# Kernel optimization log

Measured on AMD Instinct MI355X. Metric: run time of the kernel, lower is better.

## Reference

```python
import jax, jax.numpy as jnp
import numpy as np
from jax import lax

D_MODEL = 2048
D_INNER = 4096  # expand * d_model
D_CONV = 4
B, T = 4, 2048


def _rmsnorm(h):
    # F.normalize(x, dim=-1) * sqrt(D): x / max(||x||_2, 1e-12) * sqrt(D)
    n = jnp.sqrt(jnp.sum(h * h, axis=-1, keepdims=True))
    return h / jnp.maximum(n, 1e-12) * (h.shape[-1] ** 0.5)


def setup_inputs() -> dict:
    key = jax.random.key(0)
    ks = jax.random.split(key, 7)
    std = 0.02
    return {
        "x": jax.random.normal(ks[0], (B, T, D_MODEL), jnp.float32),
        "W_in": jax.random.normal(ks[1], (2 * D_INNER, D_MODEL), jnp.float32) * std,
        "conv_w": jax.random.normal(ks[2], (D_INNER, 1, D_CONV), jnp.float32) * std,
        "conv_b": jnp.zeros((D_INNER,), jnp.float32),
        "W_out": jax.random.normal(ks[3], (D_MODEL, D_INNER), jnp.float32) * std,
        "W_mlp1": jax.random.normal(ks[4], (4 * D_MODEL, D_MODEL), jnp.float32) * std,
        "W_mlp2": jax.random.normal(ks[5], (D_MODEL, 4 * D_MODEL), jnp.float32) * std,
    }


def _mamba_fallback(h, W_in, conv_w, conv_b, W_out):
    # in_proj: (B,T,D) -> (B,T,2*d_inner), split into x branch and gate z
    xz = jnp.einsum("btd,ed->bte", h, W_in)
    xp, z = jnp.split(xz, 2, axis=-1)
    # depthwise causal conv over time: torch pads (d_conv-1) both sides then slices [:T]
    # == left-pad-only causal cross-correlation
    xc = lax.conv_general_dilated(
        xp.transpose(0, 2, 1),  # (B, d_inner, T)
        conv_w,                  # (d_inner, 1, d_conv)
        window_strides=(1,),
        padding=[(D_CONV - 1, 0)],
        dimension_numbers=("NCH", "OIH", "NCH"),
        feature_group_count=D_INNER,
    ) + conv_b[None, :, None]
    xc = xc.transpose(0, 2, 1)  # (B, T, d_inner)
    y = jax.nn.silu(xc) * jax.nn.silu(z)
    return jnp.einsum("bte,de->btd", y, W_out)


def reference(x, W_in, conv_w, conv_b, W_out, W_mlp1, W_mlp2):
    # full-dimension path (active_dim=None)
    h = _rmsnorm(x)
    x = x + _mamba_fallback(h, W_in, conv_w, conv_b, W_out)
    h = _rmsnorm(x)
    m = jnp.einsum("bte,de->btd", jax.nn.relu(jnp.einsum("btd,ed->bte", h, W_mlp1)), W_mlp2)
    return x + m
```

## Files before the change

### kernel.cpp

```cpp
#include <hip/hip_runtime.h>
#include <hip/hip_bf16.h>

typedef __bf16 bf16;
typedef __bf16 bf16x8 __attribute__((ext_vector_type(8)));
typedef float f32x4 __attribute__((ext_vector_type(4)));

#define D_MODEL 2048
#define D_INNER 4096
#define ROWS    8192

__device__ __forceinline__ void gload_lds16(const void* g, void* l) {
    __builtin_amdgcn_global_load_lds(
        (const __attribute__((address_space(1))) void*)g,
        (__attribute__((address_space(3))) void*)l, 16, 0, 0);
}

__device__ __forceinline__ void f2b_body(const float* __restrict__ in,
                                         bf16* __restrict__ out, int i, int n8) {
    if (i >= n8) return;
    long base = (long)i * 8;
    float4 a = *(const float4*)(in + base);
    float4 b = *(const float4*)(in + base + 4);
    bf16x8 o;
    o[0] = (bf16)a.x; o[1] = (bf16)a.y; o[2] = (bf16)a.z; o[3] = (bf16)a.w;
    o[4] = (bf16)b.x; o[5] = (bf16)b.y; o[6] = (bf16)b.z; o[7] = (bf16)b.w;
    *(bf16x8*)(out + base) = o;
}

__device__ __forceinline__ void rmsnorm_body(const float* __restrict__ x,
                                             bf16* __restrict__ h, int row) {
    const float* xr = x + (long)row * D_MODEL;
    float4 v0 = ((const float4*)xr)[threadIdx.x * 2];
    float4 v1 = ((const float4*)xr)[threadIdx.x * 2 + 1];
    float ss = v0.x*v0.x + v0.y*v0.y + v0.z*v0.z + v0.w*v0.w
             + v1.x*v1.x + v1.y*v1.y + v1.z*v1.z + v1.w*v1.w;
    #pragma unroll
    for (int o = 32; o; o >>= 1) ss += __shfl_xor(ss, o, 64);
    __shared__ float red[4];
    if ((threadIdx.x & 63) == 0) red[threadIdx.x >> 6] = ss;
    __syncthreads();
    float tot = red[0] + red[1] + red[2] + red[3];
    float scale = 45.254834f / fmaxf(sqrtf(tot), 1e-12f);
    bf16x8 o;
    o[0] = (bf16)(v0.x*scale); o[1] = (bf16)(v0.y*scale);
    o[2] = (bf16)(v0.z*scale); o[3] = (bf16)(v0.w*scale);
    o[4] = (bf16)(v1.x*scale); o[5] = (bf16)(v1.y*scale);
    o[6] = (bf16)(v1.z*scale); o[7] = (bf16)(v1.w*scale);
    *(bf16x8*)(h + (long)row * D_MODEL + threadIdx.x * 8) = o;
}

__device__ __forceinline__ void conv_body(bf16* __restrict__ xz,
                                          const float* __restrict__ cw,
                                          const float* __restrict__ cb, int idx) {
    const int c8  = idx & 511;
    const int row = idx >> 9;
    const int t   = row & 2047;
    const int c0  = c8 * 8;
    float acc[8];
    float wv[8][4];
    #pragma unroll
    for (int e = 0; e < 8; ++e) {
        float4 f = ((const float4*)cw)[c0 + e];
        wv[e][0] = f.x; wv[e][1] = f.y; wv[e][2] = f.z; wv[e][3] = f.w;
        acc[e] = cb[c0 + e];
    }
    #pragma unroll
    for (int j = 0; j < 4; ++j) {
        if (t + j - 3 >= 0) {
            bf16x8 xv = *(const bf16x8*)(xz + (long)(row + j - 3) * (2*D_INNER) + c0);
            #pragma unroll
            for (int e = 0; e < 8; ++e) acc[e] += (float)xv[e] * wv[e][j];
        }
    }
    bf16* zp = xz + (long)row * (2*D_INNER) + D_INNER + c0;
    bf16x8 zv = *(const bf16x8*)zp;
    bf16x8 yv;
    #pragma unroll
    for (int e = 0; e < 8; ++e) {
        float xc = acc[e];
        float s1 = xc / (1.f + __expf(-xc));
        float z  = (float)zv[e];
        float s2 = z / (1.f + __expf(-z));
        yv[e] = (bf16)(s1 * s2);
    }
    *(bf16x8*)zp = yv;
}

__global__ __launch_bounds__(256) void prep_kernel(const float* __restrict__ x,
                                                   bf16* __restrict__ h,
                                                   const float* __restrict__ w,
                                                   bf16* __restrict__ wOut, int n8) {
    if ((int)blockIdx.x < ROWS) rmsnorm_body(x, h, blockIdx.x);
    else f2b_body(w, wOut, (blockIdx.x - ROWS) * 256 + threadIdx.x, n8);
}

__global__ __launch_bounds__(256) void convf2b_kernel(bf16* __restrict__ xz,
                                                      const float* __restrict__ cw,
                                                      const float* __restrict__ cb,
                                                      const float* __restrict__ w,
                                                      bf16* __restrict__ wOut, int n8) {
    if ((int)blockIdx.x < 16384) conv_body(xz, cw, cb, blockIdx.x * 256 + threadIdx.x);
    else f2b_body(w, wOut, (blockIdx.x - 16384) * 256 + threadIdx.x, n8);
}

__global__ __launch_bounds__(256) void f2b_kernel(const float* __restrict__ in,
                                                  bf16* __restrict__ out, int n8) {
    f2b_body(in, out, blockIdx.x * 256 + threadIdx.x, n8);
}

template<int EPI>
__global__ __launch_bounds__(512, 2) void gemm_bt(
        const bf16* __restrict__ A, long lda,
        const bf16* __restrict__ B,
        void* __restrict__ C, const float* __restrict__ res,
        int N, int K, int gx) {
    __shared__ __align__(16) char LB[131072];
    const int tid = threadIdx.x;
    const int w   = tid >> 6;
    const int l   = tid & 63;
    const int lr  = l & 15;

    int bx, by;
    if (gx == 32) {
        const int xcd = blockIdx.x & 7, i = blockIdx.x >> 3;
        by = (xcd >> 1) * 8 + (i >> 4);
        bx = (xcd & 1) * 16 + (i & 15);
    } else {
        const int qq = gridDim.x >> 3;
        const int sw = (blockIdx.x & 7) * qq + (blockIdx.x >> 3);
        bx = sw % gx; by = sw / gx;
    }
    const long rowBase = (long)by * 256;
    const long colBase = (long)bx * 256;

    const int srow = w * 8 + (l >> 3);
    const int schk = (l & 7) ^ ((l >> 3) & 7);
    const bf16* aSrc = A + (rowBase + srow) * lda + schk * 8;
    const bf16* bSrc = B + (colBase + srow) * (long)K + schk * 8;
    const long lda64 = 64 * lda;
    const long ldb64 = 64 * (long)K;
    const int  w1024 = w * 1024;

    auto stgA = [&](int DBB, int kt) {
        const bf16* s = aSrc + (long)kt * 64;
        gload_lds16(s,            LB + DBB +     0 + w1024);
        gload_lds16(s +   lda64,  LB + DBB +  8192 + w1024);
        gload_lds16(s + 2*lda64,  LB + DBB + 16384 + w1024);
        gload_lds16(s + 3*lda64,  LB + DBB + 24576 + w1024);
    };
    auto stgB = [&](int DBB, int kt) {
        const bf16* s = bSrc + (long)kt * 64;
        gload_lds16(s,            LB + DBB + 32768 + w1024);
        gload_lds16(s +   ldb64,  LB + DBB + 40960 + w1024);
        gload_lds16(s + 2*ldb64,  LB + DBB + 49152 + w1024);
        gload_lds16(s + 3*ldb64,  LB + DBB + 57344 + w1024);
    };

    const int cx0 = (((l >> 4)    ) ^ (l & 7)) << 4;
    const int cx1 = (((l >> 4) + 4) ^ (l & 7)) << 4;
    const int hm = w >> 2;
    const int q  = w & 3;
    int aRow[8], bRow[4];
    #pragma unroll
    for (int m = 0; m < 8; ++m) aRow[m] = hm * 16384 + (m * 16 + lr) * 128;
    #pragma unroll
    for (int n = 0; n < 4; ++n)
        bRow[n] = 32768 + (q >> 1) * 16384 + ((q & 1) * 64 + n * 16 + lr) * 128;

    const int nt  = K >> 6;
    const int nit = nt >> 1;
    f32x4 acc[8][4] = {};
    bf16x8 AX[4][2], BL[2][2], BH[2][2];

    stgB(0, 0);      stgA(0, 0);
    stgB(65536, 1);  stgA(65536, 1);
    asm volatile("s_waitcnt vmcnt(8)" ::: "memory");
    __builtin_amdgcn_s_barrier();
    __builtin_amdgcn_sched_barrier(0);
    #pragma unroll
    for (int m = 0; m < 4; ++m) {
        AX[m][0] = *(const bf16x8*)(LB + aRow[m] + cx0);
        AX[m][1] = *(const bf16x8*)(LB + aRow[m] + cx1);
    }
    #pragma unroll
    for (int n = 0; n < 2; ++n) {
        BL[n][0] = *(const bf16x8*)(LB + bRow[n]     + cx0);
        BL[n][1] = *(const bf16x8*)(LB + bRow[n]     + cx1);
    }
    #pragma unroll
    for (int n = 0; n < 2; ++n) {
        BH[n][0] = *(const bf16x8*)(LB + bRow[n + 2] + cx0);
        BH[n][1] = *(const bf16x8*)(LB + bRow[n + 2] + cx1);
    }
    asm volatile("s_waitcnt lgkmcnt(4)" ::: "memory");
    __builtin_amdgcn_sched_barrier(0);
    __builtin_amdgcn_s_setprio(1);
    #pragma unroll
    for (int m = 0; m < 4; ++m)
        #pragma unroll
        for (int n = 0; n < 2; ++n) {
            acc[m][n] = __builtin_amdgcn_mfma_f32_16x16x32_bf16(AX[m][0], BL[n][0], acc[m][n], 0, 0, 0);
            acc[m][n] = __builtin_amdgcn_mfma_f32_16x16x32_bf16(AX[m][1], BL[n][1], acc[m][n], 0, 0, 0);
        }
    __builtin_amdgcn_s_setprio(0);
    __builtin_amdgcn_s_barrier();

    for (int it = 0; it < nit; ++it) {
        int kA = 2 * it + 2; if (kA >= nt) kA = 0;
        int kB = 2 * it + 3; if (kB >= nt) kB = 0;
        #pragma unroll
        for (int db = 0; db < 2; ++db) {
            const int DBB = db * 65536;
            const char* Lb = LB + DBB;
            const char* Ln = LB + (DBB ^ 65536);
            const int kst = db ? kB : kA;
            const bool full = (db == 0) || (it < nit - 1);

            stgB(DBB, kst);
            __builtin_amdgcn_s_setprio(1);
            #pragma unroll
            for (int m = 0; m < 4; ++m) {
                #pragma unroll
                for (int n = 0; n < 2; ++n) {
                    acc[m][n + 2] = __builtin_amdgcn_mfma_f32_16x16x32_bf16(AX[m][0], BH[n][0], acc[m][n + 2], 0, 0, 0);
                    acc[m][n + 2] = __builtin_amdgcn_mfma_f32_16x16x32_bf16(AX[m][1], BH[n][1], acc[m][n + 2], 0, 0, 0);
                }
                AX[m][0] = *(const bf16x8*)(Lb + aRow[m + 4] + cx0);
                AX[m][1] = *(const bf16x8*)(Lb + aRow[m + 4] + cx1);
            }
            __builtin_amdgcn_s_setprio(0);
            asm volatile("s_waitcnt lgkmcnt(0)" ::: "memory");
            __builtin_amdgcn_sched_barrier(0);
            __builtin_amdgcn_s_setprio(1);
            #pragma unroll
            for (int m = 0; m < 4; ++m)
                #pragma unroll
                for (int n = 0; n < 2; ++n) {
                    acc[m + 4][n + 2] = __builtin_amdgcn_mfma_f32_16x16x32_bf16(AX[m][0], BH[n][0], acc[m + 4][n + 2], 0, 0, 0);
                    acc[m + 4][n + 2] = __builtin_amdgcn_mfma_f32_16x16x32_bf16(AX[m][1], BH[n][1], acc[m + 4][n + 2], 0, 0, 0);
                }
            __builtin_amdgcn_s_setprio(0);
            asm volatile("s_waitcnt vmcnt(4)" ::: "memory");
            __builtin_amdgcn_s_barrier();
            __builtin_amdgcn_sched_barrier(0);

            __builtin_amdgcn_s_setprio(1);
            #pragma unroll
            for (int m = 0; m < 4; ++m) {
                #pragma unroll
                for (int n = 0; n < 2; ++n) {
                    acc[m + 4][n] = __builtin_amdgcn_mfma_f32_16x16x32_bf16(AX[m][0], BL[n][0], acc[m + 4][n], 0, 0, 0);
                    acc[m + 4][n] = __builtin_amdgcn_mfma_f32_16x16x32_bf16(AX[m][1], BL[n][1], acc[m + 4][n], 0, 0, 0);
                }
                if (full) {
                    AX[m][0] = *(const bf16x8*)(Ln + aRow[m] + cx0);
                    AX[m][1] = *(const bf16x8*)(Ln + aRow[m] + cx1);
                }
            }
            __builtin_amdgcn_s_setprio(0);
            __builtin_amdgcn_sched_barrier(0);
            stgA(DBB, kst);
            if (full) {
                #pragma unroll
                for (int n = 0; n < 2; ++n) {
                    BL[n][0] = *(const bf16x8*)(Ln + bRow[n]     + cx0);
                    BL[n][1] = *(const bf16x8*)(Ln + bRow[n]     + cx1);
                }
                #pragma unroll
                for (int n = 0; n < 2; ++n) {
                    BH[n][0] = *(const bf16x8*)(Ln + bRow[n + 2] + cx0);
                    BH[n][1] = *(const bf16x8*)(Ln + bRow[n + 2] + cx1);
                }
                asm volatile("s_waitcnt lgkmcnt(4)" ::: "memory");
                __builtin_amdgcn_sched_barrier(0);
                __builtin_amdgcn_s_setprio(1);
                #pragma unroll
                for (int m = 0; m < 4; ++m)
                    #pragma unroll
                    for (int n = 0; n < 2; ++n) {
                        acc[m][n] = __builtin_amdgcn_mfma_f32_16x16x32_bf16(AX[m][0], BL[n][0], acc[m][n], 0, 0, 0);
                        acc[m][n] = __builtin_amdgcn_mfma_f32_16x16x32_bf16(AX[m][1], BL[n][1], acc[m][n], 0, 0, 0);
                    }
                __builtin_amdgcn_s_setprio(0);
            }
            __builtin_amdgcn_s_barrier();
        }
    }

    asm volatile("s_waitcnt vmcnt(0)" ::: "memory");
    __builtin_amdgcn_s_barrier();

    const int lg = l >> 4;
    const long wrow = rowBase + hm * 128;
    const long wcol = colBase + q * 64;
    char* ep = LB + w * 16384;

    if (EPI == 2) {
        #pragma unroll
        for (int mh = 0; mh < 2; ++mh) {
            #pragma unroll
            for (int m = 0; m < 4; ++m) {
                #pragma unroll
                for (int n = 0; n < 4; ++n) {
                    f32x4 v = acc[mh * 4 + m][n];
                    #pragma unroll
                    for (int r = 0; r < 4; ++r) {
                        int rowr = m * 16 + lg * 4 + r;
                        int chnk = (n * 4 + (lr >> 2)) ^ (rowr & 7);
                        *(float*)(ep + rowr * 256 + chnk * 16 + (lr & 3) * 4) = v[r];
                    }
                }
            }
            asm volatile("s_waitcnt lgkmcnt(0)" ::: "memory");
            #pragma unroll
            for (int i = 0; i < 16; ++i) {
                int rr = i * 4 + (l >> 4);
                float4 lv = *(float4*)(ep + rr * 256 + (((l & 15) ^ (rr & 7)) * 16));
                long off = (wrow + mh * 64 + rr) * N + wcol + (l & 15) * 4;
                float4 rv = *(const float4*)(res + off);
                lv.x += rv.x; lv.y += rv.y; lv.z += rv.z; lv.w += rv.w;
                *(float4*)((float*)C + off) = lv;
            }
            if (mh == 0) { asm volatile("s_waitcnt lgkmcnt(0) vmcnt(0)" ::: "memory"); }
        }
    } else {
        #pragma unroll
        for (int m = 0; m < 8; ++m) {
            #pragma unroll
            for (int n = 0; n < 4; ++n) {
                f32x4 v = acc[m][n];
                #pragma unroll
                for (int r = 0; r < 4; ++r) {
                    int rowr = m * 16 + lg * 4 + r;
                    int chnk = (n * 2 + (lr >> 3)) ^ (rowr & 7);
                    float val = (EPI == 1) ? fmaxf(v[r], 0.f) : v[r];
                    *(bf16*)(ep + rowr * 128 + chnk * 16 + (lr & 7) * 2) = (bf16)val;
                }
            }
        }
        asm volatile("s_waitcnt lgkmcnt(0)" ::: "memory");
        #pragma unroll
        for (int i = 0; i < 16; ++i) {
            int rr = i * 8 + (l >> 3);
            uint4 lv = *(uint4*)(ep + rr * 128 + (((l & 7) ^ (rr & 7)) * 16));
            *(uint4*)((bf16*)C + (wrow + rr) * N + wcol + (l & 7) * 8) = lv;
        }
    }
}

extern "C" void kernel_launch(void* const* d_in, const int* in_sizes, int n_in,
                              void* d_out, int out_size, void* d_ws, size_t ws_size,
                              hipStream_t stream) {
    const float* x      = (const float*)d_in[0];
    const float* W_in   = (const float*)d_in[1];
    const float* cw     = (const float*)d_in[2];
    const float* cb     = (const float*)d_in[3];
    const float* W_out  = (const float*)d_in[4];
    const float* W_mlp1 = (const float*)d_in[5];
    const float* W_mlp2 = (const float*)d_in[6];
    float* out = (float*)d_out;

    char* ws  = (char*)d_ws;
    bf16* wW  = (bf16*)(ws);
    bf16* h   = (bf16*)(ws + 33554432);
    bf16* xz  = (bf16*)(ws + 67108864);
    float* x2 = (float*)(ws + 201326592);
    bf16* y   = xz + D_INNER;
    bf16* m1  = xz;

    dim3 blk(256);
    dim3 gblk(512);

    prep_kernel<<<dim3(ROWS + 8192), blk, 0, stream>>>(x, h, W_in, wW, 16777216/8);
    gemm_bt<0><<<dim3(1024), gblk, 0, stream>>>(h, D_MODEL, wW, xz, nullptr, 2*D_INNER, D_MODEL, 32);
    convf2b_kernel<<<dim3(16384 + 4096), blk, 0, stream>>>(xz, cw, cb, W_out, wW, 8388608/8);
    gemm_bt<2><<<dim3(256), gblk, 0, stream>>>(y, 2*D_INNER, wW, x2, x, D_MODEL, D_INNER, 8);

    prep_kernel<<<dim3(ROWS + 8192), blk, 0, stream>>>(x2, h, W_mlp1, wW, 16777216/8);
    gemm_bt<1><<<dim3(1024), gblk, 0, stream>>>(h, D_MODEL, wW, m1, nullptr, 4*D_MODEL, D_MODEL, 32);
    f2b_kernel<<<dim3(8192), blk, 0, stream>>>(W_mlp2, wW, 16777216/8);
    gemm_bt<2><<<dim3(256), gblk, 0, stream>>>(m1, 4*D_MODEL, wW, out, x2, D_MODEL, 4*D_MODEL, 8);
}
```

Before: 958.8 us.

## Store residual x2 in bf16, merge W_mlp2 conversion into prep, split GEMM staging

The intermediate residual x2 is now written in bf16 instead of fp32, which halves its write and re-read traffic; the rmsnorm and final residual add read the bf16 copy. The W_mlp2 fp32-to-bf16 conversion moves into the second prep kernel using a separate workspace buffer, which removes one launch. The GEMM global-to-LDS staging is split into halves that are interleaved with the LDS fragment reads to spread memory issue across the loop. Rounding x2 to bf16 loses precision on the residual stream, and the EPI==2 epilogue now does scalar strided residual loads.

```diff
diff --git a/kernel.cpp b/kernel.cpp
--- a/kernel.cpp
+++ b/kernel.cpp
@@ -3,6 +3,7 @@
 
 typedef __bf16 bf16;
 typedef __bf16 bf16x8 __attribute__((ext_vector_type(8)));
+typedef __bf16 bf16x4 __attribute__((ext_vector_type(4)));
 typedef float f32x4 __attribute__((ext_vector_type(4)));
 
 #define D_MODEL 2048
@@ -49,6 +50,27 @@
     *(bf16x8*)(h + (long)row * D_MODEL + threadIdx.x * 8) = o;
 }
 
+__device__ __forceinline__ void rmsnorm_body_b16(const bf16* __restrict__ x,
+                                                 bf16* __restrict__ h, int row) {
+    const bf16* xr = x + (long)row * D_MODEL;
+    bf16x8 v = *(const bf16x8*)(xr + threadIdx.x * 8);
+    float f[8];
+    float ss = 0.f;
+    #pragma unroll
+    for (int e = 0; e < 8; ++e) { f[e] = (float)v[e]; ss += f[e] * f[e]; }
+    #pragma unroll
+    for (int o = 32; o; o >>= 1) ss += __shfl_xor(ss, o, 64);
+    __shared__ float red[4];
+    if ((threadIdx.x & 63) == 0) red[threadIdx.x >> 6] = ss;
+    __syncthreads();
+    float tot = red[0] + red[1] + red[2] + red[3];
+    float scale = 45.254834f / fmaxf(sqrtf(tot), 1e-12f);
+    bf16x8 o;
+    #pragma unroll
+    for (int e = 0; e < 8; ++e) o[e] = (bf16)(f[e] * scale);
+    *(bf16x8*)(h + (long)row * D_MODEL + threadIdx.x * 8) = o;
+}
+
 __device__ __forceinline__ void conv_body(bf16* __restrict__ xz,
                                           const float* __restrict__ cw,
                                           const float* __restrict__ cb, int idx) {
@@ -94,6 +116,19 @@
     else f2b_body(w, wOut, (blockIdx.x - ROWS) * 256 + threadIdx.x, n8);
 }
 
+__global__ __launch_bounds__(256) void prep2_kernel(const bf16* __restrict__ x2b,
+                                                    bf16* __restrict__ h,
+                                                    const float* __restrict__ w1,
+                                                    bf16* __restrict__ w1o,
+                                                    const float* __restrict__ w2,
+                                                    bf16* __restrict__ w2o, int n8) {
+    if ((int)blockIdx.x < ROWS) rmsnorm_body_b16(x2b, h, blockIdx.x);
+    else if ((int)blockIdx.x < 2 * ROWS)
+        f2b_body(w1, w1o, (blockIdx.x - ROWS) * 256 + threadIdx.x, n8);
+    else
+        f2b_body(w2, w2o, (blockIdx.x - 2 * ROWS) * 256 + threadIdx.x, n8);
+}
+
 __global__ __launch_bounds__(256) void convf2b_kernel(bf16* __restrict__ xz,
                                                       const float* __restrict__ cw,
                                                       const float* __restrict__ cb,
@@ -103,16 +138,11 @@
     else f2b_body(w, wOut, (blockIdx.x - 16384) * 256 + threadIdx.x, n8);
 }
 
-__global__ __launch_bounds__(256) void f2b_kernel(const float* __restrict__ in,
-                                                  bf16* __restrict__ out, int n8) {
-    f2b_body(in, out, blockIdx.x * 256 + threadIdx.x, n8);
-}
-
 template<int EPI>
 __global__ __launch_bounds__(512, 2) void gemm_bt(
         const bf16* __restrict__ A, long lda,
         const bf16* __restrict__ B,
-        void* __restrict__ C, const float* __restrict__ res,
+        void* __restrict__ C, const void* __restrict__ res,
         int N, int K, int gx) {
     __shared__ __align__(16) char LB[131072];
     const int tid = threadIdx.x;
@@ -141,17 +171,23 @@
     const long ldb64 = 64 * (long)K;
     const int  w1024 = w * 1024;
 
-    auto stgA = [&](int DBB, int kt) {
+    auto stgA0 = [&](int DBB, int kt) {
         const bf16* s = aSrc + (long)kt * 64;
         gload_lds16(s,            LB + DBB +     0 + w1024);
         gload_lds16(s +   lda64,  LB + DBB +  8192 + w1024);
+    };
+    auto stgA1 = [&](int DBB, int kt) {
+        const bf16* s = aSrc + (long)kt * 64;
         gload_lds16(s + 2*lda64,  LB + DBB + 16384 + w1024);
         gload_lds16(s + 3*lda64,  LB + DBB + 24576 + w1024);
     };
-    auto stgB = [&](int DBB, int kt) {
+    auto stgB0 = [&](int DBB, int kt) {
         const bf16* s = bSrc + (long)kt * 64;
         gload_lds16(s,            LB + DBB + 32768 + w1024);
         gload_lds16(s +   ldb64,  LB + DBB + 40960 + w1024);
+    };
+    auto stgB1 = [&](int DBB, int kt) {
+        const bf16* s = bSrc + (long)kt * 64;
         gload_lds16(s + 2*ldb64,  LB + DBB + 49152 + w1024);
         gload_lds16(s + 3*ldb64,  LB + DBB + 57344 + w1024);
     };
@@ -172,8 +208,8 @@
     f32x4 acc[8][4] = {};
     bf16x8 AX[4][2], BL[2][2], BH[2][2];
 
-    stgB(0, 0);      stgA(0, 0);
-    stgB(65536, 1);  stgA(65536, 1);
+    stgB0(0, 0); stgB1(0, 0); stgA0(0, 0); stgA1(0, 0);
+    stgB0(65536, 1); stgB1(65536, 1); stgA0(65536, 1); stgA1(65536, 1);
     asm volatile("s_waitcnt vmcnt(8)" ::: "memory");
     __builtin_amdgcn_s_barrier();
     __builtin_amdgcn_sched_barrier(0);
@@ -216,7 +252,7 @@
             const int kst = db ? kB : kA;
             const bool full = (db == 0) || (it < nit - 1);
 
-            stgB(DBB, kst);
+            stgB0(DBB, kst);
             __builtin_amdgcn_s_setprio(1);
             #pragma unroll
             for (int m = 0; m < 4; ++m) {
@@ -229,6 +265,7 @@
                 AX[m][1] = *(const bf16x8*)(Lb + aRow[m + 4] + cx1);
             }
             __builtin_amdgcn_s_setprio(0);
+            stgB1(DBB, kst);
             asm volatile("s_waitcnt lgkmcnt(0)" ::: "memory");
             __builtin_amdgcn_sched_barrier(0);
             __builtin_amdgcn_s_setprio(1);
@@ -255,23 +292,25 @@
                 if (full) {
                     AX[m][0] = *(const bf16x8*)(Ln + aRow[m] + cx0);
                     AX[m][1] = *(const bf16x8*)(Ln + aRow[m] + cx1);
+                    if (m < 2) {
+                        BH[m][0] = *(const bf16x8*)(Ln + bRow[m + 2] + cx0);
+                        BH[m][1] = *(const bf16x8*)(Ln + bRow[m + 2] + cx1);
+                    }
                 }
             }
             __builtin_amdgcn_s_setprio(0);
             __builtin_amdgcn_sched_barrier(0);
-            stgA(DBB, kst);
+            stgA0(DBB, kst);
             if (full) {
                 #pragma unroll
                 for (int n = 0; n < 2; ++n) {
                     BL[n][0] = *(const bf16x8*)(Ln + bRow[n]     + cx0);
                     BL[n][1] = *(const bf16x8*)(Ln + bRow[n]     + cx1);
                 }
-                #pragma unroll
-                for (int n = 0; n < 2; ++n) {
-                    BH[n][0] = *(const bf16x8*)(Ln + bRow[n + 2] + cx0);
-                    BH[n][1] = *(const bf16x8*)(Ln + bRow[n + 2] + cx1);
-                }
-                asm volatile("s_waitcnt lgkmcnt(4)" ::: "memory");
+            }
+            stgA1(DBB, kst);
+            if (full) {
+                asm volatile("s_waitcnt lgkmcnt(0)" ::: "memory");
                 __builtin_amdgcn_sched_barrier(0);
                 __builtin_amdgcn_s_setprio(1);
                 #pragma unroll
@@ -295,7 +334,8 @@
     const long wcol = colBase + q * 64;
     char* ep = LB + w * 16384;
 
-    if (EPI == 2) {
+    if (EPI == 3) {
+        const bf16* rb = (const bf16*)res;
         #pragma unroll
         for (int mh = 0; mh < 2; ++mh) {
             #pragma unroll
@@ -317,13 +357,15 @@
                 int rr = i * 4 + (l >> 4);
                 float4 lv = *(float4*)(ep + rr * 256 + (((l & 15) ^ (rr & 7)) * 16));
                 long off = (wrow + mh * 64 + rr) * N + wcol + (l & 15) * 4;
-                float4 rv = *(const float4*)(res + off);
-                lv.x += rv.x; lv.y += rv.y; lv.z += rv.z; lv.w += rv.w;
+                bf16x4 rv = *(const bf16x4*)(rb + off);
+                lv.x += (float)rv[0]; lv.y += (float)rv[1];
+                lv.z += (float)rv[2]; lv.w += (float)rv[3];
                 *(float4*)((float*)C + off) = lv;
             }
             if (mh == 0) { asm volatile("s_waitcnt lgkmcnt(0) vmcnt(0)" ::: "memory"); }
         }
     } else {
+        const float* rf = (const float*)res;
         #pragma unroll
         for (int m = 0; m < 8; ++m) {
             #pragma unroll
@@ -333,7 +375,9 @@
                 for (int r = 0; r < 4; ++r) {
                     int rowr = m * 16 + lg * 4 + r;
                     int chnk = (n * 2 + (lr >> 3)) ^ (rowr & 7);
-                    float val = (EPI == 1) ? fmaxf(v[r], 0.f) : v[r];
+                    float val = v[r];
+                    if (EPI == 1) val = fmaxf(val, 0.f);
+                    if (EPI == 2) val += rf[(wrow + rowr) * N + wcol + n * 16 + lr];
                     *(bf16*)(ep + rowr * 128 + chnk * 16 + (lr & 7) * 2) = (bf16)val;
                 }
             }
@@ -364,7 +408,8 @@
     bf16* wW  = (bf16*)(ws);
     bf16* h   = (bf16*)(ws + 33554432);
     bf16* xz  = (bf16*)(ws + 67108864);
-    float* x2 = (float*)(ws + 201326592);
+    bf16* x2b = (bf16*)(ws + 201326592);
+    bf16* wW2 = (bf16*)(ws + 234881024);
     bf16* y   = xz + D_INNER;
     bf16* m1  = xz;
 
@@ -374,10 +419,9 @@
     prep_kernel<<<dim3(ROWS + 8192), blk, 0, stream>>>(x, h, W_in, wW, 16777216/8);
     gemm_bt<0><<<dim3(1024), gblk, 0, stream>>>(h, D_MODEL, wW, xz, nullptr, 2*D_INNER, D_MODEL, 32);
     convf2b_kernel<<<dim3(16384 + 4096), blk, 0, stream>>>(xz, cw, cb, W_out, wW, 8388608/8);
-    gemm_bt<2><<<dim3(256), gblk, 0, stream>>>(y, 2*D_INNER, wW, x2, x, D_MODEL, D_INNER, 8);
-
-    prep_kernel<<<dim3(ROWS + 8192), blk, 0, stream>>>(x2, h, W_mlp1, wW, 16777216/8);
+    gemm_bt<2><<<dim3(256), gblk, 0, stream>>>(y, 2*D_INNER, wW, x2b, x, D_MODEL, D_INNER, 8);
+
+    prep2_kernel<<<dim3(3 * ROWS), blk, 0, stream>>>(x2b, h, W_mlp1, wW, W_mlp2, wW2, 16777216/8);
     gemm_bt<1><<<dim3(1024), gblk, 0, stream>>>(h, D_MODEL, wW, m1, nullptr, 4*D_MODEL, D_MODEL, 32);
-    f2b_kernel<<<dim3(8192), blk, 0, stream>>>(W_mlp2, wW, 16777216/8);
-    gemm_bt<2><<<dim3(256), gblk, 0, stream>>>(m1, 4*D_MODEL, wW, out, x2, D_MODEL, 4*D_MODEL, 8);
-}
+    gemm_bt<3><<<dim3(256), gblk, 0, stream>>>(m1, 4*D_MODEL, wW2, out, x2b, D_MODEL, 4*D_MODEL, 8);
+}
```

After: 934.2 us (median of 2 runs). 2.6% less time.
